# Kernel tuning notes

Measured on AMD Instinct MI355X. Metric: run time of the kernel, lower is better.

Reference implementation:

```python
import jax, jax.numpy as jnp
import numpy as np

B, T, V, E, H = 256, 64, 10000, 512, 1024

def setup_inputs() -> dict:
    key = jax.random.key(0)
    ks = jax.random.split(key, 8)
    seq = jax.random.randint(ks[0], (B, T), 0, V)
    seq_len = jax.random.randint(ks[1], (B, 1), 1, T + 1)
    seq_len = seq_len.at[0, 0].set(T)  # ensure max length == T (output time dim)
    std = 1.0 / np.sqrt(H)
    u = lambda k, s: jax.random.uniform(k, s, jnp.float32, -std, std)
    embed = jax.random.normal(ks[2], (V, E), jnp.float32) * 0.02
    x2h_w = u(ks[3], (E, 4 * H)); x2h_b = u(ks[4], (4 * H,))
    h2h_w = u(ks[5], (H, 4 * H)); h2h_b = u(ks[6], (4 * H,))
    aff_w = jax.random.uniform(ks[7], (H, H), jnp.float32, -std, std)
    aff_b = jnp.zeros((H,), jnp.float32)
    return {"seq": seq, "seq_len": seq_len, "embed": embed,
            "x2h_w": x2h_w, "x2h_b": x2h_b, "h2h_w": h2h_w, "h2h_b": h2h_b,
            "aff_w": aff_w, "aff_b": aff_b}


def reference(seq, seq_len, embed, x2h_w, x2h_b, h2h_w, h2h_b, aff_w, aff_b):
    b, t = seq.shape
    h_dim = h2h_w.shape[0]
    lens = seq_len[:, 0]                                   # [B]
    valid = jnp.arange(t)[None, :] < lens[:, None]         # [B,T] True where step is in-sequence
    x = embed[seq]                                         # [B,T,E]
    # Precompute input-to-hidden projection for all timesteps (one big GEMM).
    xg = jnp.einsum('bte,eg->btg', x, x2h_w) + x2h_b       # [B,T,4H]

    def step(carry, inp):
        h, c = carry
        xg_t, v_t = inp                                    # [B,4H], [B]
        gates = xg_t + h @ h2h_w + h2h_b
        i, f, g, o = jnp.split(gates, 4, axis=1)           # torch chunk order: in, forget, new_mem, out
        c_new = jax.nn.sigmoid(f) * c + jax.nn.sigmoid(i) * jnp.tanh(g)
        h_new = jax.nn.sigmoid(o) * jnp.tanh(c_new)
        v = v_t[:, None]
        # frozen state past each sequence's length (batch shrinks in torch loop)
        h2 = jnp.where(v, h_new, h)
        c2 = jnp.where(v, c_new, c)
        # recorded states are zero past the length (preallocated zeros in torch)
        return (h2, c2), (jnp.where(v, h_new, 0.0), jnp.where(v, c_new, 0.0))

    h0 = jnp.zeros((b, h_dim), xg.dtype)
    c0 = jnp.zeros((b, h_dim), xg.dtype)
    (h_last, _), (hs, cs) = jax.lax.scan(
        step, (h0, c0), (xg.transpose(1, 0, 2), valid.T))
    hidden_states = hs.transpose(1, 0, 2)                  # [B,T,H]
    memory_states = cs.transpose(1, 0, 2)                  # [B,T,H]
    final_hidden = jnp.tanh(h_last @ aff_w + aff_b)        # h at last valid step per sequence
    mask = valid.astype(jnp.float32)                       # == (memory_states.sum(2) != 0)
    return hidden_states, memory_states, final_hidden, mask
```

## Files before the change

kernel.cpp:

```cpp
#include <hip/hip_runtime.h>

#define B_ 256
#define T_ 64
#define V_ 10000
#define E_ 512
#define H_ 1024
#define G_ 4096
#define NWG_ 256

typedef __attribute__((ext_vector_type(8))) short short8;
typedef __attribute__((ext_vector_type(4))) float f32x4;

static __device__ __forceinline__ float bf2f(unsigned short u) {
    return __uint_as_float(((unsigned int)u) << 16);
}
static __device__ __forceinline__ unsigned short f2bf(float f) {
    unsigned int i = __float_as_uint(f);
    unsigned int r = (i + 0x7FFFu + ((i >> 16) & 1u)) >> 16;
    return (unsigned short)r;
}
static __device__ __forceinline__ float sigmoid_f(float x) {
    return 1.0f / (1.0f + __expf(-x));
}
static __device__ __forceinline__ float tanh_f(float x) {
    return 1.0f - 2.0f / (__expf(2.0f * x) + 1.0f);
}
static __device__ __forceinline__ unsigned int f2fp8(float f) {
    int pk = __builtin_amdgcn_cvt_pk_fp8_f32(f, f, 0, false);
    return (unsigned int)(pk & 0xFF);
}

static __device__ __forceinline__ void gload16(const void* g, void* l) {
    __builtin_amdgcn_global_load_lds((const __attribute__((address_space(1))) void*)g,
                                     (__attribute__((address_space(3))) void*)l, 16, 0, 0);
}

#define LD8C(dst, ptr) \
    asm volatile("global_load_dwordx2 %0, %1, off sc0 sc1" : "=v"(dst) : "v"(ptr))
#define DRAIN() do { asm volatile("s_waitcnt vmcnt(0)" ::: "memory"); \
                     __builtin_amdgcn_sched_barrier(0); } while (0)
#define STBYTEC(ptr, val) \
    asm volatile("global_store_byte %0, %1, off sc0 sc1" :: "v"(ptr), "v"(val) : "memory")
#define STDWC(ptr, val) \
    asm volatile("global_store_dword %0, %1, off sc0 sc1" :: "v"(ptr), "v"(val) : "memory")

static __device__ __forceinline__ unsigned ld_u32_cohere(const void* p) {
    unsigned r;
    asm volatile("global_load_dword %0, %1, off sc0 sc1\n\ts_waitcnt vmcnt(0)"
                 : "=v"(r) : "v"(p) : "memory");
    return r;
}

__global__ __launch_bounds__(256) void k_cvt(const float* __restrict__ in,
                                             unsigned short* __restrict__ out, int n4) {
    int i = blockIdx.x * 256 + threadIdx.x;
    if (i >= n4) return;
    float4 v = reinterpret_cast<const float4*>(in)[i];
    uint2 p;
    p.x = (unsigned int)f2bf(v.x) | ((unsigned int)f2bf(v.y) << 16);
    p.y = (unsigned int)f2bf(v.z) | ((unsigned int)f2bf(v.w) << 16);
    reinterpret_cast<uint2*>(out)[i] = p;
}

__global__ __launch_bounds__(256) void k_cvt8(const unsigned short* __restrict__ in,
                                              unsigned char* __restrict__ out, int n2) {
    int i = blockIdx.x * 256 + threadIdx.x;
    if (i >= n2) return;
    unsigned int p = reinterpret_cast<const unsigned int*>(in)[i];
    float a = bf2f((unsigned short)(p & 0xFFFF));
    float b = bf2f((unsigned short)(p >> 16));
    int pk = __builtin_amdgcn_cvt_pk_fp8_f32(a, b, 0, false);
    reinterpret_cast<unsigned short*>(out)[i] = (unsigned short)(pk & 0xFFFF);
}

__global__ __launch_bounds__(256) void k_transpose(const float* __restrict__ w,
                                                   unsigned short* __restrict__ wT,
                                                   int K, int N) {
    __shared__ float tile[32][33];
    int nblk = N >> 5;
    int bx = blockIdx.x % nblk;
    int by = blockIdx.x / nblk;
    int lx = threadIdx.x & 31;
    int ly = threadIdx.x >> 5;
    int k0 = by * 32, n0 = bx * 32;
#pragma unroll
    for (int i = 0; i < 32; i += 8)
        tile[ly + i][lx] = w[(size_t)(k0 + ly + i) * N + n0 + lx];
    __syncthreads();
#pragma unroll
    for (int i = 0; i < 32; i += 8)
        wT[(size_t)(n0 + ly + i) * K + k0 + lx] = f2bf(tile[lx][ly + i]);
}

__global__ __launch_bounds__(256) void k_xg(const int* __restrict__ seq,
                                            const unsigned short* __restrict__ emb,
                                            const unsigned short* __restrict__ wT,
                                            const float* __restrict__ bias,
                                            unsigned short* __restrict__ xg) {
    const int mt = blockIdx.x & 127;
    const int nt = blockIdx.x >> 7;
    const int tid = threadIdx.x;
    const int w = tid >> 6, l = tid & 63, g = l >> 4, li = l & 15;
    const int wr = w >> 1, wc = w & 1;

    __shared__ unsigned short As[128 * 32];
    __shared__ unsigned short Bs[128 * 32];
    __shared__ int seqv[128];

    if (tid < 128) seqv[tid] = seq[mt * 128 + tid];
    __syncthreads();

    const int r0 = w * 16 + (l >> 2);
    const int kc = (l & 3) * 8;
    const unsigned short* asrc0 = emb + (size_t)seqv[r0] * E_ + kc;
    const unsigned short* asrc1 = emb + (size_t)seqv[r0 + 64] * E_ + kc;
    const unsigned short* bsrc0 = wT + (size_t)(nt * 128 + r0) * E_ + kc;
    const unsigned short* bsrc1 = wT + (size_t)(nt * 128 + r0 + 64) * E_ + kc;
    char* aldsw = (char*)As + w * 1024;
    char* bldsw = (char*)Bs + w * 1024;

    f32x4 acc[4][4] = {};
    for (int k0 = 0; k0 < E_; k0 += 32) {
        gload16(asrc0 + k0, aldsw);
        gload16(asrc1 + k0, aldsw + 4096);
        gload16(bsrc0 + k0, bldsw);
        gload16(bsrc1 + k0, bldsw + 4096);
        __syncthreads();
        short8 af[4], bf[4];
#pragma unroll
        for (int i = 0; i < 4; ++i) {
            af[i] = *(const short8*)(As + (wr * 64 + i * 16 + li) * 32 + g * 8);
            bf[i] = *(const short8*)(Bs + (wc * 64 + i * 16 + li) * 32 + g * 8);
        }
#pragma unroll
        for (int i = 0; i < 4; ++i)
#pragma unroll
            for (int j = 0; j < 4; ++j)
                acc[i][j] = __builtin_amdgcn_mfma_f32_16x16x32_bf16(af[i], bf[j], acc[i][j], 0, 0, 0);
        __syncthreads();
    }

#pragma unroll
    for (int j = 0; j < 4; ++j) {
        const int col = nt * 128 + wc * 64 + j * 16 + li;
        const float bv = bias[col];
#pragma unroll
        for (int i = 0; i < 4; ++i) {
            const int row = mt * 128 + wr * 64 + i * 16 + g * 4;
#pragma unroll
            for (int r = 0; r < 4; ++r)
                xg[(size_t)(row + r) * G_ + col] = f2bf(acc[i][j][r] + bv);
        }
    }
}

__global__ __launch_bounds__(256) void k_rnn(const unsigned short* __restrict__ xg,
                                             const unsigned char* __restrict__ wT8,
                                             const float* __restrict__ bias,
                                             const int* __restrict__ seq_len,
                                             unsigned char* __restrict__ h80,
                                             unsigned char* __restrict__ h81,
                                             unsigned short* __restrict__ hb,
                                             float* __restrict__ hs,
                                             float* __restrict__ cs,
                                             unsigned int* __restrict__ flags) {
    const int wg = blockIdx.x;
    const int rb = wg >> 6, cb = wg & 63;
    const int tid = threadIdx.x;
    const int w = tid >> 6, l = tid & 63, g = l >> 4, li = l & 15;

    __shared__ unsigned char Bs8[64 * 1024];

    for (int gi = 0; gi < 32; ++gi) {
        int gidx = gi * 256 + tid;
        int ls = gidx & 63;
        int frag = gidx >> 6;
        int kk = frag & 31, q = frag >> 5;
        int col = q * 1024 + cb * 16 + (ls & 15);
        const unsigned char* src = wT8 + (size_t)col * H_ + kk * 32 + (ls >> 4) * 8;
        *(long*)(Bs8 + (size_t)gidx * 8) = *(const long*)src;
    }

    const int hc = cb * 16 + li;
    float bv[4];
#pragma unroll
    for (int q = 0; q < 4; ++q) bv[q] = bias[q * 1024 + hc];
    const int m0 = rb * 64 + w * 16 + g * 4;
    int sl[4];
#pragma unroll
    for (int r = 0; r < 4; ++r) sl[r] = seq_len[m0 + r];
    float creg[4] = {0.f, 0.f, 0.f, 0.f};
    float hreg[4] = {0.f, 0.f, 0.f, 0.f};

    const int arow_i = rb * 64 + w * 16 + li;
    const unsigned char* bbase = Bs8 + l * 8;
    const unsigned int* fp = flags + (rb << 6) + tid;

    __syncthreads();

#define LOADS(buf, c) do { _Pragma("unroll") \
    for (int p = 0; p < 8; ++p) LD8C(buf[p], arow8 + ((c) + p) * 32); } while (0)

#define MFMAS(buf, c) do { _Pragma("unroll") \
    for (int p = 0; p < 8; ++p) { \
        const int kk = (c) + p; \
        _Pragma("unroll") \
        for (int q = 0; q < 4; ++q) { \
            long bfv = *(const long*)(bbase + (((q * 32 + kk)) << 9)); \
            acc[q] = __builtin_amdgcn_mfma_f32_16x16x32_fp8_fp8(buf[p], bfv, acc[q], 0, 0, 0); \
        } } } while (0)

    unsigned short xgr[4][4];
#pragma unroll
    for (int r = 0; r < 4; ++r) {
        const size_t xoff = ((size_t)(m0 + r) * T_ + 0) * G_ + hc;
#pragma unroll
        for (int q = 0; q < 4; ++q) xgr[r][q] = xg[xoff + q * 1024];
    }
    asm volatile("" ::: "memory");

    for (int t = 0; t < T_; ++t) {
        const unsigned char* h_in = (t & 1) ? h81 : h80;
        unsigned char* h_out = (t & 1) ? h80 : h81;
        const unsigned char* arow8 = h_in + (size_t)arow_i * H_ + g * 8;

        f32x4 acc[4] = {};
        long A0[8], A1[8];
        LOADS(A0, 0);
        DRAIN();
        LOADS(A1, 8);
        MFMAS(A0, 0);
        DRAIN();
        LOADS(A0, 16);
        MFMAS(A1, 8);
        DRAIN();
        LOADS(A1, 24);
        MFMAS(A0, 16);
        DRAIN();
        MFMAS(A1, 24);

        float hsv[4], csv[4];
#pragma unroll
        for (int r = 0; r < 4; ++r) {
            const int m = m0 + r;
            float ig = sigmoid_f(acc[0][r] + bv[0] + bf2f(xgr[r][0]));
            float fg = sigmoid_f(acc[1][r] + bv[1] + bf2f(xgr[r][1]));
            float gg = tanh_f(acc[2][r] + bv[2] + bf2f(xgr[r][2]));
            float og = sigmoid_f(acc[3][r] + bv[3] + bf2f(xgr[r][3]));
            float cn = fg * creg[r] + ig * gg;
            float hn = og * tanh_f(cn);
            bool valid = t < sl[r];
            if (valid) { creg[r] = cn; hreg[r] = hn; }
            hsv[r] = valid ? hn : 0.0f;
            csv[r] = valid ? cn : 0.0f;
            STBYTEC(h_out + (size_t)m * H_ + hc, f2fp8(hreg[r]));
        }

        DRAIN();
        __syncthreads();
        const unsigned int tp1 = (unsigned int)(t + 1);
        if (tid == 0) {
            STDWC(flags + wg, tp1);
        }

#pragma unroll
        for (int r = 0; r < 4; ++r) {
            const size_t ooff = ((size_t)(m0 + r) * T_ + t) * H_ + hc;
            __builtin_nontemporal_store(hsv[r], &hs[ooff]);
            __builtin_nontemporal_store(csv[r], &cs[ooff]);
        }

        if (t < T_ - 1) {
#pragma unroll
            for (int r = 0; r < 4; ++r) {
                const size_t xoff = ((size_t)(m0 + r) * T_ + (t + 1)) * G_ + hc;
#pragma unroll
                for (int q = 0; q < 4; ++q) xgr[r][q] = xg[xoff + q * 1024];
            }
            asm volatile("" ::: "memory");
            if (tid < 64) {
                while (ld_u32_cohere(fp) < tp1) __builtin_amdgcn_s_sleep(1);
            }
            __syncthreads();
        }
    }
#undef LOADS
#undef MFMAS

#pragma unroll
    for (int r = 0; r < 4; ++r)
        hb[(size_t)(m0 + r) * H_ + hc] = f2bf(hreg[r]);
}

__global__ __launch_bounds__(256) void k_final(const unsigned short* __restrict__ h,
                                               const unsigned short* __restrict__ wT,
                                               const float* __restrict__ bias,
                                               float* __restrict__ fin) {
    const int rb = blockIdx.x & 3;
    const int nb = blockIdx.x >> 2;
    const int tid = threadIdx.x;
    const int w = tid >> 6;
    const int l = tid & 63;
    const int g = l >> 4, li = l & 15;

    __shared__ unsigned short As[64][40];
    __shared__ unsigned short Bs[64][40];

    const int srow = tid >> 2;
    const int scol = (tid & 3) * 8;
    const unsigned short* aptr = h + (size_t)(rb * 64 + srow) * H_ + scol;
    const unsigned short* bptr = wT + (size_t)(nb * 64 + srow) * H_ + scol;

    f32x4 acc[4] = {};
    int4 ra = *(const int4*)aptr;
    int4 rb2 = *(const int4*)bptr;
    for (int kk = 0; kk < H_; kk += 32) {
        *(int4*)&As[srow][scol] = ra;
        *(int4*)&Bs[srow][scol] = rb2;
        __syncthreads();
        if (kk + 32 < H_) {
            ra = *(const int4*)(aptr + kk + 32);
            rb2 = *(const int4*)(bptr + kk + 32);
        }
        short8 af = *(const short8*)&As[w * 16 + li][g * 8];
#pragma unroll
        for (int q = 0; q < 4; ++q) {
            short8 bf = *(const short8*)&Bs[q * 16 + li][g * 8];
            acc[q] = __builtin_amdgcn_mfma_f32_16x16x32_bf16(af, bf, acc[q], 0, 0, 0);
        }
        __syncthreads();
    }
    const int m0 = rb * 64 + w * 16 + g * 4;
#pragma unroll
    for (int q = 0; q < 4; ++q) {
        int col = nb * 64 + q * 16 + li;
        float bv = bias[col];
#pragma unroll
        for (int r = 0; r < 4; ++r)
            fin[(size_t)(m0 + r) * H_ + col] = tanh_f(acc[q][r] + bv);
    }
}

__global__ __launch_bounds__(256) void k_mask(const int* __restrict__ seq_len,
                                              float* __restrict__ mask) {
    int i = blockIdx.x * 256 + threadIdx.x;
    int b = i >> 6, t = i & 63;
    mask[i] = (t < seq_len[b]) ? 1.0f : 0.0f;
}

extern "C" void kernel_launch(void* const* d_in, const int* in_sizes, int n_in,
                              void* d_out, int out_size, void* d_ws, size_t ws_size,
                              hipStream_t stream) {
    const int* seq = (const int*)d_in[0];
    const int* seq_len = (const int*)d_in[1];
    const float* embed = (const float*)d_in[2];
    const float* x2h_w = (const float*)d_in[3];
    const float* x2h_b = (const float*)d_in[4];
    const float* h2h_w = (const float*)d_in[5];
    const float* h2h_b = (const float*)d_in[6];
    const float* aff_w = (const float*)d_in[7];
    const float* aff_b = (const float*)d_in[8];

    float* out = (float*)d_out;
    float* hs = out;
    float* cs = out + (size_t)B_ * T_ * H_;
    float* fin = cs + (size_t)B_ * T_ * H_;
    float* mask = fin + (size_t)B_ * H_;

    char* p = (char*)d_ws;
    unsigned short* emb_b = (unsigned short*)p; p += (size_t)V_ * E_ * 2;
    unsigned short* x2h_t = (unsigned short*)p; p += (size_t)G_ * E_ * 2;
    unsigned short* h2h_t = (unsigned short*)p; p += (size_t)G_ * H_ * 2;
    unsigned char*  h2h_8 = (unsigned char*)p;  p += (size_t)G_ * H_;
    unsigned short* aff_t = (unsigned short*)p; p += (size_t)H_ * H_ * 2;
    unsigned short* xg    = (unsigned short*)p; p += (size_t)B_ * T_ * G_ * 2;
    unsigned char*  h8b0  = (unsigned char*)p;  p += (size_t)B_ * H_;
    unsigned char*  h8b1  = (unsigned char*)p;  p += (size_t)B_ * H_;
    unsigned short* hbuf  = (unsigned short*)p; p += (size_t)B_ * H_ * 2;
    unsigned int*   flags = (unsigned int*)p;   p += NWG_ * sizeof(unsigned int);

    hipLaunchKernelGGL(k_cvt, dim3((V_ * E_ / 4 + 255) / 256), dim3(256), 0, stream,
                       embed, emb_b, V_ * E_ / 4);
    hipLaunchKernelGGL(k_transpose, dim3((E_ / 32) * (G_ / 32)), dim3(256), 0, stream,
                       x2h_w, x2h_t, E_, G_);
    hipLaunchKernelGGL(k_transpose, dim3((H_ / 32) * (G_ / 32)), dim3(256), 0, stream,
                       h2h_w, h2h_t, H_, G_);
    hipLaunchKernelGGL(k_cvt8, dim3((G_ * H_ / 2 + 255) / 256), dim3(256), 0, stream,
                       h2h_t, h2h_8, G_ * H_ / 2);
    hipLaunchKernelGGL(k_transpose, dim3((H_ / 32) * (H_ / 32)), dim3(256), 0, stream,
                       aff_w, aff_t, H_, H_);

    hipLaunchKernelGGL(k_xg, dim3(128 * 32), dim3(256), 0, stream,
                       seq, emb_b, x2h_t, x2h_b, xg);

    hipMemsetAsync(h8b0, 0, (size_t)B_ * H_, stream);
    hipMemsetAsync(flags, 0, NWG_ * sizeof(unsigned int), stream);

    {
        const unsigned short* xg_p = xg;
        const unsigned char* wT8_p = h2h_8;
        const float* b_p = h2h_b;
        const int* sl_p = seq_len;
        unsigned char* h80_p = h8b0;
        unsigned char* h81_p = h8b1;
        unsigned short* hb_p = hbuf;
        float* hs_p = hs;
        float* cs_p = cs;
        unsigned int* fl_p = flags;
        void* args[] = {(void*)&xg_p, (void*)&wT8_p, (void*)&b_p, (void*)&sl_p,
                        (void*)&h80_p, (void*)&h81_p, (void*)&hb_p,
                        (void*)&hs_p, (void*)&cs_p, (void*)&fl_p};
        hipLaunchCooperativeKernel(reinterpret_cast<void*>(k_rnn), dim3(NWG_), dim3(256),
                                   args, 0, stream);
    }

    hipLaunchKernelGGL(k_final, dim3(64), dim3(256), 0, stream, hbuf, aff_t, aff_b, fin);
    hipLaunchKernelGGL(k_mask, dim3(B_ * T_ / 256), dim3(256), 0, stream, seq_len, mask);
}
```

Baseline: 665.6 us.

## Use per-timestep hidden buffers to allow cached loads; fuse transpose with fp8 cast

Replaces the ping-pong fp8 hidden-state buffers with a distinct buffer per timestep. Each location is then written once, so the recurrent kernel can read h with ordinary cached loads instead of coherent sc0 sc1 loads. The h2h weight transpose and fp8 conversion are fused into one kernel, removing an intermediate bf16 buffer and a launch. This uses more workspace and relies on cache coherence assumptions for the newly written lines.

Result: faster. 612.6 us (-8.0%).

```diff
diff --git a/kernel.cpp b/kernel.cpp
--- a/kernel.cpp
+++ b/kernel.cpp
@@ -35,8 +35,6 @@
                                      (__attribute__((address_space(3))) void*)l, 16, 0, 0);
 }
 
-#define LD8C(dst, ptr) \
-    asm volatile("global_load_dwordx2 %0, %1, off sc0 sc1" : "=v"(dst) : "v"(ptr))
 #define DRAIN() do { asm volatile("s_waitcnt vmcnt(0)" ::: "memory"); \
                      __builtin_amdgcn_sched_barrier(0); } while (0)
 #define STBYTEC(ptr, val) \
@@ -60,17 +58,6 @@
     p.x = (unsigned int)f2bf(v.x) | ((unsigned int)f2bf(v.y) << 16);
     p.y = (unsigned int)f2bf(v.z) | ((unsigned int)f2bf(v.w) << 16);
     reinterpret_cast<uint2*>(out)[i] = p;
-}
-
-__global__ __launch_bounds__(256) void k_cvt8(const unsigned short* __restrict__ in,
-                                              unsigned char* __restrict__ out, int n2) {
-    int i = blockIdx.x * 256 + threadIdx.x;
-    if (i >= n2) return;
-    unsigned int p = reinterpret_cast<const unsigned int*>(in)[i];
-    float a = bf2f((unsigned short)(p & 0xFFFF));
-    float b = bf2f((unsigned short)(p >> 16));
-    int pk = __builtin_amdgcn_cvt_pk_fp8_f32(a, b, 0, false);
-    reinterpret_cast<unsigned short*>(out)[i] = (unsigned short)(pk & 0xFFFF);
 }
 
 __global__ __launch_bounds__(256) void k_transpose(const float* __restrict__ w,
@@ -92,6 +79,25 @@
         wT[(size_t)(n0 + ly + i) * K + k0 + lx] = f2bf(tile[lx][ly + i]);
 }
 
+__global__ __launch_bounds__(256) void k_transpose8(const float* __restrict__ w,
+                                                    unsigned char* __restrict__ wT,
+                                                    int K, int N) {
+    __shared__ float tile[32][33];
+    int nblk = N >> 5;
+    int bx = blockIdx.x % nblk;
+    int by = blockIdx.x / nblk;
+    int lx = threadIdx.x & 31;
+    int ly = threadIdx.x >> 5;
+    int k0 = by * 32, n0 = bx * 32;
+#pragma unroll
+    for (int i = 0; i < 32; i += 8)
+        tile[ly + i][lx] = w[(size_t)(k0 + ly + i) * N + n0 + lx];
+    __syncthreads();
+#pragma unroll
+    for (int i = 0; i < 32; i += 8)
+        wT[(size_t)(n0 + ly + i) * K + k0 + lx] = (unsigned char)f2fp8(tile[lx][ly + i]);
+}
+
 __global__ __launch_bounds__(256) void k_xg(const int* __restrict__ seq,
                                             const unsigned short* __restrict__ emb,
                                             const unsigned short* __restrict__ wT,
@@ -158,8 +164,7 @@
                                              const unsigned char* __restrict__ wT8,
                                              const float* __restrict__ bias,
                                              const int* __restrict__ seq_len,
-                                             unsigned char* __restrict__ h80,
-                                             unsigned char* __restrict__ h81,
+                                             unsigned char* __restrict__ h8,
                                              unsigned short* __restrict__ hb,
                                              float* __restrict__ hs,
                                              float* __restrict__ cs,
@@ -199,7 +204,7 @@
     __syncthreads();
 
 #define LOADS(buf, c) do { _Pragma("unroll") \
-    for (int p = 0; p < 8; ++p) LD8C(buf[p], arow8 + ((c) + p) * 32); } while (0)
+    for (int p = 0; p < 8; ++p) buf[p] = *(const long*)(arow8 + ((c) + p) * 32); } while (0)
 
 #define MFMAS(buf, c) do { _Pragma("unroll") \
     for (int p = 0; p < 8; ++p) { \
@@ -220,8 +225,8 @@
     asm volatile("" ::: "memory");
 
     for (int t = 0; t < T_; ++t) {
-        const unsigned char* h_in = (t & 1) ? h81 : h80;
-        unsigned char* h_out = (t & 1) ? h80 : h81;
+        const unsigned char* h_in = h8 + (size_t)t * (B_ * H_);
+        unsigned char* h_out = (unsigned char*)h8 + (size_t)(t + 1) * (B_ * H_);
         const unsigned char* arow8 = h_in + (size_t)arow_i * H_ + g * 8;
 
         f32x4 acc[4] = {};
@@ -370,12 +375,10 @@
     char* p = (char*)d_ws;
     unsigned short* emb_b = (unsigned short*)p; p += (size_t)V_ * E_ * 2;
     unsigned short* x2h_t = (unsigned short*)p; p += (size_t)G_ * E_ * 2;
-    unsigned short* h2h_t = (unsigned short*)p; p += (size_t)G_ * H_ * 2;
     unsigned char*  h2h_8 = (unsigned char*)p;  p += (size_t)G_ * H_;
     unsigned short* aff_t = (unsigned short*)p; p += (size_t)H_ * H_ * 2;
     unsigned short* xg    = (unsigned short*)p; p += (size_t)B_ * T_ * G_ * 2;
-    unsigned char*  h8b0  = (unsigned char*)p;  p += (size_t)B_ * H_;
-    unsigned char*  h8b1  = (unsigned char*)p;  p += (size_t)B_ * H_;
+    unsigned char*  h8    = (unsigned char*)p;  p += (size_t)(T_ + 1) * B_ * H_;
     unsigned short* hbuf  = (unsigned short*)p; p += (size_t)B_ * H_ * 2;
     unsigned int*   flags = (unsigned int*)p;   p += NWG_ * sizeof(unsigned int);
 
@@ -383,17 +386,15 @@
                        embed, emb_b, V_ * E_ / 4);
     hipLaunchKernelGGL(k_transpose, dim3((E_ / 32) * (G_ / 32)), dim3(256), 0, stream,
                        x2h_w, x2h_t, E_, G_);
-    hipLaunchKernelGGL(k_transpose, dim3((H_ / 32) * (G_ / 32)), dim3(256), 0, stream,
-                       h2h_w, h2h_t, H_, G_);
-    hipLaunchKernelGGL(k_cvt8, dim3((G_ * H_ / 2 + 255) / 256), dim3(256), 0, stream,
-                       h2h_t, h2h_8, G_ * H_ / 2);
+    hipLaunchKernelGGL(k_transpose8, dim3((H_ / 32) * (G_ / 32)), dim3(256), 0, stream,
+                       h2h_w, h2h_8, H_, G_);
     hipLaunchKernelGGL(k_transpose, dim3((H_ / 32) * (H_ / 32)), dim3(256), 0, stream,
                        aff_w, aff_t, H_, H_);
 
     hipLaunchKernelGGL(k_xg, dim3(128 * 32), dim3(256), 0, stream,
                        seq, emb_b, x2h_t, x2h_b, xg);
 
-    hipMemsetAsync(h8b0, 0, (size_t)B_ * H_, stream);
+    hipMemsetAsync(h8, 0, (size_t)B_ * H_, stream);
     hipMemsetAsync(flags, 0, NWG_ * sizeof(unsigned int), stream);
 
     {
@@ -401,14 +402,13 @@
         const unsigned char* wT8_p = h2h_8;
         const float* b_p = h2h_b;
         const int* sl_p = seq_len;
-        unsigned char* h80_p = h8b0;
-        unsigned char* h81_p = h8b1;
+        unsigned char* h8_p = h8;
         unsigned short* hb_p = hbuf;
         float* hs_p = hs;
         float* cs_p = cs;
         unsigned int* fl_p = flags;
         void* args[] = {(void*)&xg_p, (void*)&wT8_p, (void*)&b_p, (void*)&sl_p,
-                        (void*)&h80_p, (void*)&h81_p, (void*)&hb_p,
+                        (void*)&h8_p, (void*)&hb_p,
                         (void*)&hs_p, (void*)&cs_p, (void*)&fl_p};
         hipLaunchCooperativeKernel(reinterpret_cast<void*>(k_rnn), dim3(NWG_), dim3(256),
                                    args, 0, stream);
```
